# Kernel optimization log

Measured on AMD Instinct MI355X. Metric: run time of the kernel, lower is better.

The kernel has to match this reference:

```python
import jax, jax.numpy as jnp
import numpy as np

GRID_MIN = -2.0
GRID_MAX = 2.0
NUM_GRIDS = 8
IN_DIM = 512
OUT_DIM = 512
N = 16384
SPLINE_SCALE = 0.1


def setup_inputs() -> dict:
    key = jax.random.key(0)
    k_x, k_sw, k_w, k_b = jax.random.split(key, 4)
    x = jax.random.normal(k_x, (N, IN_DIM), dtype=jnp.float32)
    grid = jnp.linspace(GRID_MIN, GRID_MAX, NUM_GRIDS, dtype=jnp.float32)
    spline_weight = jax.random.normal(k_sw, (IN_DIM * NUM_GRIDS, OUT_DIM), dtype=jnp.float32) * SPLINE_SCALE
    bound = 1.0 / np.sqrt(IN_DIM)
    base_w = jax.random.uniform(k_w, (OUT_DIM, IN_DIM), minval=-bound, maxval=bound, dtype=jnp.float32)
    base_b = jax.random.uniform(k_b, (OUT_DIM,), minval=-bound, maxval=bound, dtype=jnp.float32)
    return {"x": x, "grid": grid, "spline_weight": spline_weight, "base_w": base_w, "base_b": base_b}


def reference(x, grid, spline_weight, base_w, base_b):
    # Gaussian RBF basis over the grid: (N, in_dim, num_grids)
    h = (GRID_MAX - GRID_MIN) / (NUM_GRIDS - 1)  # grid spacing
    basis = jnp.exp(-(((x[..., None] - grid) / h) ** 2))
    ret = basis.reshape(x.shape[0], -1) @ spline_weight  # (N, out_dim)
    base = jax.nn.silu(x) @ base_w.T + base_b
    return ret + base
```

## Files before the change

kernel.cpp:

```cpp
#include <hip/hip_runtime.h>
#include <hip/hip_bf16.h>

typedef __attribute__((ext_vector_type(8))) short short8;
typedef __attribute__((ext_vector_type(4))) float floatx4;

#define N_ROWS   16384
#define IN_DIM   512
#define OUT_DIM  512
#define K_SPLINE 4096
#define K_TOT    4608
#define NKT      72
#define NPER     36
#define NSPER    32
#define NKTILE   144
#define L2E      1.4426950408889634f
#define C2E      0.13533528323661270f

__device__ __forceinline__ unsigned short f2bf(float f) {
    unsigned int u = __float_as_uint(f);
    unsigned int r = u + 0x7FFFu + ((u >> 16) & 1u);
    return (unsigned short)(r >> 16);
}

__device__ __forceinline__ unsigned packtrunc(float f0, float f1) {
    return __builtin_amdgcn_perm(__float_as_uint(f1), __float_as_uint(f0), 0x07060302);
}

__global__ __launch_bounds__(256) void prep_kernel(
    const float* __restrict__ sw, const float* __restrict__ bw,
    unsigned short* __restrict__ Btf)
{
    const int t     = threadIdx.x;
    const int lane  = t & 63;
    const int kt32  = blockIdx.x * 4 + (t >> 6);
    const int ct    = blockIdx.y;
    const int mn    = lane & 15, q = lane >> 4;
    const int n     = ct * 16 + mn;
    const int kbase = kt32 * 32 + q * 8;
    short8 v;
    if (kbase < K_SPLINE) {
        #pragma unroll
        for (int j = 0; j < 8; ++j)
            v[j] = (short)f2bf(sw[(size_t)(kbase + j) * OUT_DIM + n]);
    } else {
        #pragma unroll
        for (int j = 0; j < 8; ++j)
            v[j] = (short)f2bf(bw[(size_t)n * IN_DIM + (kbase + j - K_SPLINE)]);
    }
    reinterpret_cast<short8*>(Btf)[(size_t)(ct * NKTILE + kt32) * 64 + lane] = v;
}

__device__ __forceinline__ uint4 basis_pack(float X) {
    const float u = fmaf(1.75f, X, 3.5f);
    float b = __builtin_amdgcn_exp2f(-(u * u) * L2E);
    float r = __builtin_amdgcn_exp2f(fmaf(2.0f * L2E, u, -L2E));
    float v[8];
    v[0] = b;
    #pragma unroll
    for (int j = 1; j < 8; ++j) { b *= r; r *= C2E; v[j] = b; }
    uint4 p;
    p.x = packtrunc(v[0], v[1]);
    p.y = packtrunc(v[2], v[3]);
    p.z = packtrunc(v[4], v[5]);
    p.w = packtrunc(v[6], v[7]);
    return p;
}

__device__ __forceinline__ void stageA128(unsigned short* dst, const float* xrow,
                                          int rowA, int colq, int p, float2 xsp)
{
    unsigned short* arow = dst + rowA * 128;
    if (p < NSPER) {
        const float xv[2] = {xsp.x, xsp.y};
        #pragma unroll
        for (int e = 0; e < 2; ++e) {
            const uint4 pk = basis_pack(xv[e]);
            const int blk = (colq * 2 + e) ^ (rowA & 15);
            *reinterpret_cast<uint4*>(arow + blk * 8) = pk;
        }
    } else {
        const float* xs = xrow + (p - NSPER) * 128 + colq * 16;
        #pragma unroll
        for (int e = 0; e < 2; ++e) {
            const float4 a0 = *reinterpret_cast<const float4*>(xs + e * 8);
            const float4 a1 = *reinterpret_cast<const float4*>(xs + e * 8 + 4);
            const float f[8] = {a0.x, a0.y, a0.z, a0.w, a1.x, a1.y, a1.z, a1.w};
            float s[8];
            #pragma unroll
            for (int j = 0; j < 8; ++j)
                s[j] = f[j] * __builtin_amdgcn_rcpf(
                    1.0f + __builtin_amdgcn_exp2f(-f[j] * L2E));
            uint4 pk;
            pk.x = packtrunc(s[0], s[1]);
            pk.y = packtrunc(s[2], s[3]);
            pk.z = packtrunc(s[4], s[5]);
            pk.w = packtrunc(s[6], s[7]);
            const int blk = (colq * 2 + e) ^ (rowA & 15);
            *reinterpret_cast<uint4*>(arow + blk * 8) = pk;
        }
    }
}

template<bool PREP>
__device__ __forceinline__ void load_bfrags(short8 dst[4][2], const short8* __restrict__ Bf,
                                            const size_t* bbase, int kt,
                                            const float* __restrict__ sw,
                                            const float* __restrict__ bw,
                                            int col0, int lane)
{
    if (kt >= NKT) return;
    if (PREP) {
        #pragma unroll
        for (int nt = 0; nt < 4; ++nt)
            #pragma unroll
            for (int s = 0; s < 2; ++s)
                dst[nt][s] = Bf[bbase[nt] + (size_t)(kt * 2 + s) * 64];
    } else {
        const int mn = lane & 15, q = lane >> 4;
        #pragma unroll
        for (int nt = 0; nt < 4; ++nt) {
            const int n = col0 + nt * 16 + mn;
            #pragma unroll
            for (int s = 0; s < 2; ++s) {
                short8 v;
                #pragma unroll
                for (int j = 0; j < 8; ++j) {
                    const int k = (kt * 2 + s) * 32 + q * 8 + j;
                    const float val = (k < K_SPLINE)
                        ? sw[(size_t)k * OUT_DIM + n]
                        : bw[(size_t)n * IN_DIM + (k - K_SPLINE)];
                    v[j] = (short)f2bf(val);
                }
                dst[nt][s] = v;
            }
        }
    }
}

template<bool PREP>
__global__ __launch_bounds__(512, 2) void kan_kernel(
    const float* __restrict__ x,
    const unsigned short* __restrict__ Btf,
    const float* __restrict__ sw,
    const float* __restrict__ bw,
    const float* __restrict__ bias,
    float* __restrict__ out)
{
    __shared__ unsigned short Als[2][64 * 128];

    const int tid  = threadIdx.x;
    const int wn   = tid >> 6;
    const int lane = tid & 63;
    const int q    = lane >> 4;
    const int mn   = lane & 15;
    const int bid  = blockIdx.x;
    const int row0 = bid * 64;
    const int col0 = wn * 64;

    const int rowA = tid >> 3;
    const int colq = tid & 7;
    const float* xrow = x + (size_t)(row0 + rowA) * IN_DIM;

    size_t bbase[4];
    #pragma unroll
    for (int nt = 0; nt < 4; ++nt)
        bbase[nt] = (size_t)(((col0 >> 4) + nt) * NKTILE) * 64 + lane;
    const short8* Bf = reinterpret_cast<const short8*>(Btf);

    floatx4 acc[4][4];
    #pragma unroll
    for (int i = 0; i < 4; ++i)
        #pragma unroll
        for (int j = 0; j < 4; ++j)
            acc[i][j] = (floatx4){0.f, 0.f, 0.f, 0.f};

    short8 bb[2][4][2];

    float2 xsp = *reinterpret_cast<const float2*>(xrow + colq * 2);
    stageA128(&Als[0][0], xrow, rowA, colq, 0, xsp);
    load_bfrags<PREP>(bb[0], Bf, bbase, 0, sw, bw, col0, lane);
    xsp = *reinterpret_cast<const float2*>(xrow + 16 + colq * 2);
    __syncthreads();

    for (int p = 0; p < NPER; ++p) {
        const unsigned short* Acur = &Als[p & 1][0];
        unsigned short*       Anxt = &Als[(p & 1) ^ 1][0];

        load_bfrags<PREP>(bb[1], Bf, bbase, 2 * p + 1, sw, bw, col0, lane);

        if (p + 1 < NPER) {
            stageA128(Anxt, xrow, rowA, colq, p + 1, xsp);
            if (p + 2 < NSPER)
                xsp = *reinterpret_cast<const float2*>(
                    xrow + (p + 2) * 16 + colq * 2);
        }

        #pragma unroll
        for (int hh = 0; hh < 2; ++hh) {
            #pragma unroll
            for (int s = 0; s < 2; ++s) {
                const int st = hh * 2 + s;
                short8 af[4];
                #pragma unroll
                for (int mt = 0; mt < 4; ++mt) {
                    const int r = mt * 16 + mn;
                    af[mt] = *reinterpret_cast<const short8*>(
                        Acur + r * 128 + (((st * 4 + q) ^ (r & 15)) * 8));
                }
                #pragma unroll
                for (int mt = 0; mt < 4; ++mt)
                    #pragma unroll
                    for (int nt = 0; nt < 4; ++nt)
                        acc[mt][nt] = __builtin_amdgcn_mfma_f32_16x16x32_bf16(
                            af[mt], bb[hh][nt][s], acc[mt][nt], 0, 0, 0);
            }
            if (hh == 0)
                load_bfrags<PREP>(bb[0], Bf, bbase, 2 * p + 2, sw, bw, col0, lane);
        }
        __syncthreads();
    }

    #pragma unroll
    for (int nt = 0; nt < 4; ++nt) {
        const int col = col0 + nt * 16 + mn;
        const float bv = bias[col];
        #pragma unroll
        for (int mt = 0; mt < 4; ++mt) {
            const int rb = row0 + mt * 16 + q * 4;
            #pragma unroll
            for (int e = 0; e < 4; ++e)
                out[(size_t)(rb + e) * OUT_DIM + col] = acc[mt][nt][e] + bv;
        }
    }
}

extern "C" void kernel_launch(void* const* d_in, const int* in_sizes, int n_in,
                              void* d_out, int out_size, void* d_ws, size_t ws_size,
                              hipStream_t stream)
{
    const float* x    = (const float*)d_in[0];
    const float* sw   = (const float*)d_in[2];
    const float* bw   = (const float*)d_in[3];
    const float* bias = (const float*)d_in[4];
    float* out = (float*)d_out;

    const size_t bt_bytes = (size_t)OUT_DIM * K_TOT * sizeof(unsigned short);
    if (ws_size >= bt_bytes) {
        unsigned short* Btf = (unsigned short*)d_ws;
        prep_kernel<<<dim3(NKTILE / 4, OUT_DIM / 16), 256, 0, stream>>>(sw, bw, Btf);
        kan_kernel<true><<<dim3(256), 512, 0, stream>>>(
            x, Btf, sw, bw, bias, out);
    } else {
        kan_kernel<false><<<dim3(256), 512, 0, stream>>>(
            x, nullptr, sw, bw, bias, out);
    }
}
```

Before: 156.6 us.

## Halve rows per block to 32 and double block count with higher occupancy

Shrinks each workgroup's row tile from 64 to 32 rows, so the grid grows from 256 to 512 blocks and the machine's compute units are better covered. Each thread now stages one basis/silu packet instead of two, the accumulator array halves, and launch bounds ask for 4 blocks per CU to raise occupancy. The cost is that every block streams the entire B matrix again for half as many rows, doubling B-fragment traffic per output and halving MFMA reuse of each loaded B fragment.

```diff
diff --git a/kernel.cpp b/kernel.cpp
--- a/kernel.cpp
+++ b/kernel.cpp
@@ -13,6 +13,7 @@
 #define NPER     36
 #define NSPER    32
 #define NKTILE   144
+#define ROWS_B   32
 #define L2E      1.4426950408889634f
 #define C2E      0.13533528323661270f
 
@@ -66,38 +67,30 @@
     return p;
 }
 
-__device__ __forceinline__ void stageA128(unsigned short* dst, const float* xrow,
-                                          int rowA, int colq, int p, float2 xsp)
+__device__ __forceinline__ void stageA32(unsigned short* dst, const float* xrow,
+                                         int rowA, int colq, int p, float xsp)
 {
     unsigned short* arow = dst + rowA * 128;
+    const int blk = colq ^ (rowA & 15);
     if (p < NSPER) {
-        const float xv[2] = {xsp.x, xsp.y};
-        #pragma unroll
-        for (int e = 0; e < 2; ++e) {
-            const uint4 pk = basis_pack(xv[e]);
-            const int blk = (colq * 2 + e) ^ (rowA & 15);
-            *reinterpret_cast<uint4*>(arow + blk * 8) = pk;
-        }
-    } else {
-        const float* xs = xrow + (p - NSPER) * 128 + colq * 16;
-        #pragma unroll
-        for (int e = 0; e < 2; ++e) {
-            const float4 a0 = *reinterpret_cast<const float4*>(xs + e * 8);
-            const float4 a1 = *reinterpret_cast<const float4*>(xs + e * 8 + 4);
-            const float f[8] = {a0.x, a0.y, a0.z, a0.w, a1.x, a1.y, a1.z, a1.w};
-            float s[8];
-            #pragma unroll
-            for (int j = 0; j < 8; ++j)
-                s[j] = f[j] * __builtin_amdgcn_rcpf(
-                    1.0f + __builtin_amdgcn_exp2f(-f[j] * L2E));
-            uint4 pk;
-            pk.x = packtrunc(s[0], s[1]);
-            pk.y = packtrunc(s[2], s[3]);
-            pk.z = packtrunc(s[4], s[5]);
-            pk.w = packtrunc(s[6], s[7]);
-            const int blk = (colq * 2 + e) ^ (rowA & 15);
-            *reinterpret_cast<uint4*>(arow + blk * 8) = pk;
-        }
+        const uint4 pk = basis_pack(xsp);
+        *reinterpret_cast<uint4*>(arow + blk * 8) = pk;
+    } else {
+        const float* xs = xrow + (p - NSPER) * 128 + colq * 8;
+        const float4 a0 = *reinterpret_cast<const float4*>(xs);
+        const float4 a1 = *reinterpret_cast<const float4*>(xs + 4);
+        const float f[8] = {a0.x, a0.y, a0.z, a0.w, a1.x, a1.y, a1.z, a1.w};
+        float s[8];
+        #pragma unroll
+        for (int j = 0; j < 8; ++j)
+            s[j] = f[j] * __builtin_amdgcn_rcpf(
+                1.0f + __builtin_amdgcn_exp2f(-f[j] * L2E));
+        uint4 pk;
+        pk.x = packtrunc(s[0], s[1]);
+        pk.y = packtrunc(s[2], s[3]);
+        pk.z = packtrunc(s[4], s[5]);
+        pk.w = packtrunc(s[6], s[7]);
+        *reinterpret_cast<uint4*>(arow + blk * 8) = pk;
     }
 }
 
@@ -138,7 +131,7 @@
 }
 
 template<bool PREP>
-__global__ __launch_bounds__(512, 2) void kan_kernel(
+__global__ __launch_bounds__(512, 4) void kan_kernel(
     const float* __restrict__ x,
     const unsigned short* __restrict__ Btf,
     const float* __restrict__ sw,
@@ -146,7 +139,7 @@
     const float* __restrict__ bias,
     float* __restrict__ out)
 {
-    __shared__ unsigned short Als[2][64 * 128];
+    __shared__ unsigned short Als[2][ROWS_B * 128];
 
     const int tid  = threadIdx.x;
     const int wn   = tid >> 6;
@@ -154,11 +147,11 @@
     const int q    = lane >> 4;
     const int mn   = lane & 15;
     const int bid  = blockIdx.x;
-    const int row0 = bid * 64;
+    const int row0 = bid * ROWS_B;
     const int col0 = wn * 64;
 
-    const int rowA = tid >> 3;
-    const int colq = tid & 7;
+    const int rowA = tid >> 4;
+    const int colq = tid & 15;
     const float* xrow = x + (size_t)(row0 + rowA) * IN_DIM;
 
     size_t bbase[4];
@@ -167,19 +160,19 @@
         bbase[nt] = (size_t)(((col0 >> 4) + nt) * NKTILE) * 64 + lane;
     const short8* Bf = reinterpret_cast<const short8*>(Btf);
 
-    floatx4 acc[4][4];
-    #pragma unroll
-    for (int i = 0; i < 4; ++i)
+    floatx4 acc[2][4];
+    #pragma unroll
+    for (int i = 0; i < 2; ++i)
         #pragma unroll
         for (int j = 0; j < 4; ++j)
             acc[i][j] = (floatx4){0.f, 0.f, 0.f, 0.f};
 
     short8 bb[2][4][2];
 
-    float2 xsp = *reinterpret_cast<const float2*>(xrow + colq * 2);
-    stageA128(&Als[0][0], xrow, rowA, colq, 0, xsp);
+    float xsp = xrow[colq];
+    stageA32(&Als[0][0], xrow, rowA, colq, 0, xsp);
     load_bfrags<PREP>(bb[0], Bf, bbase, 0, sw, bw, col0, lane);
-    xsp = *reinterpret_cast<const float2*>(xrow + 16 + colq * 2);
+    xsp = xrow[16 + colq];
     __syncthreads();
 
     for (int p = 0; p < NPER; ++p) {
@@ -189,10 +182,9 @@
         load_bfrags<PREP>(bb[1], Bf, bbase, 2 * p + 1, sw, bw, col0, lane);
 
         if (p + 1 < NPER) {
-            stageA128(Anxt, xrow, rowA, colq, p + 1, xsp);
+            stageA32(Anxt, xrow, rowA, colq, p + 1, xsp);
             if (p + 2 < NSPER)
-                xsp = *reinterpret_cast<const float2*>(
-                    xrow + (p + 2) * 16 + colq * 2);
+                xsp = xrow[(p + 2) * 16 + colq];
         }
 
         #pragma unroll
@@ -200,15 +192,15 @@
             #pragma unroll
             for (int s = 0; s < 2; ++s) {
                 const int st = hh * 2 + s;
-                short8 af[4];
+                short8 af[2];
                 #pragma unroll
-                for (int mt = 0; mt < 4; ++mt) {
+                for (int mt = 0; mt < 2; ++mt) {
                     const int r = mt * 16 + mn;
                     af[mt] = *reinterpret_cast<const short8*>(
                         Acur + r * 128 + (((st * 4 + q) ^ (r & 15)) * 8));
                 }
                 #pragma unroll
-                for (int mt = 0; mt < 4; ++mt)
+                for (int mt = 0; mt < 2; ++mt)
                     #pragma unroll
                     for (int nt = 0; nt < 4; ++nt)
                         acc[mt][nt] = __builtin_amdgcn_mfma_f32_16x16x32_bf16(
@@ -225,7 +217,7 @@
         const int col = col0 + nt * 16 + mn;
         const float bv = bias[col];
         #pragma unroll
-        for (int mt = 0; mt < 4; ++mt) {
+        for (int mt = 0; mt < 2; ++mt) {
             const int rb = row0 + mt * 16 + q * 4;
             #pragma unroll
             for (int e = 0; e < 4; ++e)
@@ -248,10 +240,10 @@
     if (ws_size >= bt_bytes) {
         unsigned short* Btf = (unsigned short*)d_ws;
         prep_kernel<<<dim3(NKTILE / 4, OUT_DIM / 16), 256, 0, stream>>>(sw, bw, Btf);
-        kan_kernel<true><<<dim3(256), 512, 0, stream>>>(
+        kan_kernel<true><<<dim3(N_ROWS / ROWS_B), 512, 0, stream>>>(
             x, Btf, sw, bw, bias, out);
     } else {
-        kan_kernel<false><<<dim3(256), 512, 0, stream>>>(
+        kan_kernel<false><<<dim3(N_ROWS / ROWS_B), 512, 0, stream>>>(
             x, nullptr, sw, bw, bias, out);
     }
 }
```

New measurement: 222.5 us. +42.1%, slower.
